# Kernel tuning notes

Measured on AMD Instinct MI355X. Metric: run time of the kernel, lower is better.

Reference implementation:

```python
import jax, jax.numpy as jnp
import numpy as np

N_NODES = 50000
N_EDGES = 1600000


def gcn_conv(h, W, b, src, dst, ew, n_nodes):
    """PyG GCNConv: linear -> add self-loops (weight 1) -> sym-norm scatter-add -> bias."""
    h = h @ W                                   # [N, out]
    loop = jnp.arange(n_nodes, dtype=src.dtype)
    s = jnp.concatenate([src, loop])            # [E+N]
    d = jnp.concatenate([dst, loop])
    w = jnp.concatenate([ew, jnp.ones((n_nodes,), dtype=h.dtype)])
    deg = jax.ops.segment_sum(w, d, num_segments=n_nodes)          # in-degree (weighted)
    dinv = jnp.where(deg > 0, jax.lax.rsqrt(deg), 0.0)
    coef = dinv[s] * w * dinv[d]                # D^-1/2 A D^-1/2 per-edge coefficient
    msg = h[s] * coef[:, None]                  # gather + scale  [E+N, out]
    out = jax.ops.segment_sum(msg, d, num_segments=n_nodes)        # scatter-add
    return out + b


def setup_inputs() -> dict:
    key = jax.random.key(0)
    ks = jax.random.split(key, 6)
    x = jax.random.normal(ks[0], (N_NODES, 256), dtype=jnp.float32)
    edge_index = jax.random.randint(ks[1], (2, N_EDGES), 0, N_NODES, dtype=jnp.int64)
    edge_weight = jax.random.uniform(ks[2], (N_EDGES,), dtype=jnp.float32)
    W1 = jax.random.normal(ks[3], (256, 128), dtype=jnp.float32) * (1.0 / np.sqrt(256))
    b1 = jnp.zeros((128,), dtype=jnp.float32)
    W2 = jax.random.normal(ks[4], (128, 64), dtype=jnp.float32) * (1.0 / np.sqrt(128))
    b2 = jnp.zeros((64,), dtype=jnp.float32)
    return {"x": x, "edge_index": edge_index, "edge_weight": edge_weight,
            "W1": W1, "b1": b1, "W2": W2, "b2": b2}


def reference(x, edge_index, edge_weight, W1, b1, W2, b2):
    src, dst = edge_index[0], edge_index[1]
    n = x.shape[0]
    h = gcn_conv(x, W1, b1, src, dst, edge_weight, n)
    h = jax.nn.relu(h)
    # dropout is identity in eval mode
    out = gcn_conv(h, W2, b2, src, dst, edge_weight, n)
    return out
```

## Files before the change

kernel.cpp:

```cpp
#include <hip/hip_runtime.h>

#define NN 50000
#define NE 1600000
#define NB 391
#define NBLK 512
#define EPB 3125
#define CAP 4608

typedef short bf16x8 __attribute__((ext_vector_type(8)));
typedef float f32x4 __attribute__((ext_vector_type(4)));

static __device__ __forceinline__ unsigned f2bf(float f) {
    union { float f; unsigned u; } v; v.f = f;
    return (v.u + 0x7FFF + ((v.u >> 16) & 1)) >> 16;
}

__global__ __launch_bounds__(256) void k1_scatter(const int* __restrict__ src,
        const int* __restrict__ dst, const float* __restrict__ ew,
        int* __restrict__ cursor, int2* __restrict__ ebuf,
        const float* __restrict__ W1, const float* __restrict__ W2,
        ushort* __restrict__ Wt1, ushort* __restrict__ Wt2) {
    int blk = blockIdx.x;
    int t = threadIdx.x;
    if (blk >= NBLK) {
        for (int idx = (blk - NBLK) * 256 + t; idx < 40960; idx += 32 * 256) {
            if (idx < 32768) {
                int k = idx >> 7, n = idx & 127;
                Wt1[n * 256 + k] = (ushort)f2bf(W1[idx]);
            } else {
                int i = idx - 32768;
                int k = i >> 6, n = i & 63;
                Wt2[n * 128 + k] = (ushort)f2bf(W2[i]);
            }
        }
        return;
    }
    __shared__ int h[NB];
    __shared__ int curs[NB];
    for (int i = t; i < NB; i += 256) h[i] = 0;
    __syncthreads();
    int base = blk * EPB;
    for (int k = t; k < EPB; k += 256)
        atomicAdd(&h[dst[base + k] >> 7], 1);
    __syncthreads();
    for (int i = t; i < NB; i += 256)
        curs[i] = i * CAP + atomicAdd(&cursor[i], h[i]);
    __syncthreads();
    for (int k = t; k < EPB; k += 256) {
        int d = dst[base + k];
        int s = src[base + k];
        float w = ew[base + k];
        int pos = atomicAdd(&curs[d >> 7], 1);
        ebuf[pos] = make_int2(s | ((d & 127) << 16), __float_as_int(w));
    }
}

__global__ __launch_bounds__(512) void p4_build(const int2* __restrict__ ebuf,
        const int* __restrict__ cursor, unsigned* __restrict__ edata,
        float* __restrict__ dinv, int2* __restrict__ rowptr2) {
    __shared__ int cnt[128], loff[128], cur[128], sd[128];
    __shared__ float deg[128];
    __shared__ int2 se[CAP];
    int bk = blockIdx.x;
    int t = threadIdx.x;
    int ebase = bk * CAP;
    int ecnt = cursor[bk];
    if (ecnt > CAP) ecnt = CAP;
    if (t < 128) { cnt[t] = 0; cur[t] = 0; deg[t] = 0.0f; }
    __syncthreads();
    for (int i = t; i < ecnt; i += 512) {
        int2 e = ebuf[ebase + i];
        se[i] = e;
        int dl = (e.x >> 16) & 127;
        atomicAdd(&cnt[dl], 1);
        atomicAdd(&deg[dl], __int_as_float(e.y));
    }
    __syncthreads();
    if (t < 128) sd[t] = cnt[t];
    __syncthreads();
    for (int off = 1; off < 128; off <<= 1) {
        int v = 0;
        if (t < 128 && t >= off) v = sd[t - off];
        __syncthreads();
        if (t < 128) sd[t] += v;
        __syncthreads();
    }
    if (t < 128) loff[t] = sd[t] - cnt[t];
    __syncthreads();
    int node = bk * 128 + t;
    if (t < 128 && node < NN) {
        dinv[node] = rsqrtf(deg[t] + 1.0f);
        int beg = ebase + loff[t];
        rowptr2[node] = make_int2(beg, beg + cnt[t]);
    }
    for (int i = t; i < ecnt; i += 512) {
        int2 e = se[i];
        int dl = (e.x >> 16) & 127;
        int slot = loff[dl] + atomicAdd(&cur[dl], 1);
        edata[ebase + slot] = (unsigned)(e.x & 0xFFFF)
                            | (f2bf(__int_as_float(e.y)) << 16);
    }
}

__global__ __launch_bounds__(256) void gemm1_kernel(const float* __restrict__ A,
        const ushort* __restrict__ Bt, ushort* __restrict__ C,
        const float* __restrict__ dinv, int M) {
    const int K = 256, N = 128;
    __shared__ __align__(16) ushort As[64][72];
    __shared__ __align__(16) ushort Bs[128][72];
    int tid = threadIdx.x;
    int bm = blockIdx.x * 64;
    int w = tid >> 6, lane = tid & 63;
    int m = lane & 15, quad = lane >> 4;
    f32x4 acc[8] = {};
    int ra = tid >> 2, ksa = (tid & 3) * 16;
    int rb = tid >> 1, ksb = (tid & 1) * 32;
    int grow = bm + ra; if (grow >= M) grow = M - 1;
    const float* ap = A + (size_t)grow * K + ksa;
    const ushort* bp = Bt + (size_t)rb * K + ksb;
    for (int k0 = 0; k0 < K; k0 += 64) {
        float4 f0 = *(const float4*)(ap + k0);
        float4 f1 = *(const float4*)(ap + k0 + 4);
        float4 f2 = *(const float4*)(ap + k0 + 8);
        float4 f3 = *(const float4*)(ap + k0 + 12);
        uint4 bv0 = *(const uint4*)(bp + k0);
        uint4 bv1 = *(const uint4*)(bp + k0 + 8);
        uint4 bv2 = *(const uint4*)(bp + k0 + 16);
        uint4 bv3 = *(const uint4*)(bp + k0 + 24);
        uint4 pa, pb;
        pa.x = f2bf(f0.x) | (f2bf(f0.y) << 16);
        pa.y = f2bf(f0.z) | (f2bf(f0.w) << 16);
        pa.z = f2bf(f1.x) | (f2bf(f1.y) << 16);
        pa.w = f2bf(f1.z) | (f2bf(f1.w) << 16);
        pb.x = f2bf(f2.x) | (f2bf(f2.y) << 16);
        pb.y = f2bf(f2.z) | (f2bf(f2.w) << 16);
        pb.z = f2bf(f3.x) | (f2bf(f3.y) << 16);
        pb.w = f2bf(f3.z) | (f2bf(f3.w) << 16);
        __syncthreads();
        *(uint4*)&As[ra][ksa] = pa;
        *(uint4*)&As[ra][ksa + 8] = pb;
        *(uint4*)&Bs[rb][ksb] = bv0;
        *(uint4*)&Bs[rb][ksb + 8] = bv1;
        *(uint4*)&Bs[rb][ksb + 16] = bv2;
        *(uint4*)&Bs[rb][ksb + 24] = bv3;
        __syncthreads();
        #pragma unroll
        for (int ks = 0; ks < 2; ++ks) {
            bf16x8 a = *(const bf16x8*)&As[w * 16 + m][ks * 32 + quad * 8];
            #pragma unroll
            for (int t = 0; t < 8; ++t) {
                bf16x8 b = *(const bf16x8*)&Bs[t * 16 + m][ks * 32 + quad * 8];
                acc[t] = __builtin_amdgcn_mfma_f32_16x16x32_bf16(a, b, acc[t], 0, 0, 0);
            }
        }
    }
    int rbase = bm + w * 16 + quad * 4;
    float dv[4];
    #pragma unroll
    for (int rg = 0; rg < 4; ++rg)
        dv[rg] = (rbase + rg < M) ? dinv[rbase + rg] : 0.0f;
    #pragma unroll
    for (int t = 0; t < 8; ++t) {
        int col = t * 16 + m;
        #pragma unroll
        for (int rg = 0; rg < 4; ++rg) {
            int row = rbase + rg;
            if (row < M)
                C[(size_t)row * N + col] = (ushort)f2bf(dv[rg] * acc[t][rg]);
        }
    }
}

__global__ __launch_bounds__(256) void agg1_fused_kernel(
        const int2* __restrict__ rowptr2, const unsigned* __restrict__ edata,
        const ushort* __restrict__ H, const float* __restrict__ dinv,
        const float* __restrict__ bias, const ushort* __restrict__ Wt2,
        ushort* __restrict__ H2) {
    __shared__ __align__(16) ushort Ats[16][136];
    int tid = threadIdx.x;
    int nl = tid >> 4;
    int node = blockIdx.x * 16 + nl;
    int glane = tid & 15;
    int gb = (tid & 63) & ~15;
    int2 rp = rowptr2[node];
    int beg = rp.x, end = rp.y;
    float acc[8] = {};
    const ushort* Hl = H + (size_t)glane * 8;
    for (int chunk = beg; chunk < end; chunk += 16) {
        int nch = end - chunk; if (nch > 16) nch = 16;
        int ed = 0;
        if (glane < nch) ed = (int)edata[chunk + glane];
        int j = 0;
        for (; j + 2 <= nch; j += 2) {
            int e0 = __shfl(ed, gb + j);
            int e1 = __shfl(ed, gb + j + 1);
            int s0 = e0 & 0xFFFF;
            int s1 = e1 & 0xFFFF;
            float c0 = __uint_as_float((unsigned)e0 & 0xFFFF0000u);
            float c1 = __uint_as_float((unsigned)e1 & 0xFFFF0000u);
            uint4 h0 = *(const uint4*)(Hl + (size_t)s0 * 128);
            uint4 h1 = *(const uint4*)(Hl + (size_t)s1 * 128);
            const unsigned* u0 = (const unsigned*)&h0;
            const unsigned* u1 = (const unsigned*)&h1;
            #pragma unroll
            for (int q = 0; q < 4; ++q) {
                acc[2*q]   += __uint_as_float(u0[q] << 16) * c0;
                acc[2*q+1] += __uint_as_float(u0[q] & 0xFFFF0000u) * c0;
            }
            #pragma unroll
            for (int q = 0; q < 4; ++q) {
                acc[2*q]   += __uint_as_float(u1[q] << 16) * c1;
                acc[2*q+1] += __uint_as_float(u1[q] & 0xFFFF0000u) * c1;
            }
        }
        if (j < nch) {
            int e0 = __shfl(ed, gb + j);
            int s0 = e0 & 0xFFFF;
            float c0 = __uint_as_float((unsigned)e0 & 0xFFFF0000u);
            uint4 h0 = *(const uint4*)(Hl + (size_t)s0 * 128);
            const unsigned* u0 = (const unsigned*)&h0;
            #pragma unroll
            for (int q = 0; q < 4; ++q) {
                acc[2*q]   += __uint_as_float(u0[q] << 16) * c0;
                acc[2*q+1] += __uint_as_float(u0[q] & 0xFFFF0000u) * c0;
            }
        }
    }
    float di = dinv[node];
    uint4 hn = *(const uint4*)(Hl + (size_t)node * 128);
    const unsigned* un = (const unsigned*)&hn;
    float4 bv0 = *(const float4*)(bias + glane * 8);
    float4 bv1 = *(const float4*)(bias + glane * 8 + 4);
    float v[8];
    #pragma unroll
    for (int q = 0; q < 4; ++q) {
        v[2*q]   = di * (acc[2*q]   + __uint_as_float(un[q] << 16));
        v[2*q+1] = di * (acc[2*q+1] + __uint_as_float(un[q] & 0xFFFF0000u));
    }
    v[0] += bv0.x; v[1] += bv0.y; v[2] += bv0.z; v[3] += bv0.w;
    v[4] += bv1.x; v[5] += bv1.y; v[6] += bv1.z; v[7] += bv1.w;
    #pragma unroll
    for (int k = 0; k < 8; ++k) v[k] = fmaxf(v[k], 0.0f);
    uint4 o;
    o.x = f2bf(v[0]) | (f2bf(v[1]) << 16);
    o.y = f2bf(v[2]) | (f2bf(v[3]) << 16);
    o.z = f2bf(v[4]) | (f2bf(v[5]) << 16);
    o.w = f2bf(v[6]) | (f2bf(v[7]) << 16);
    *(uint4*)&Ats[nl][glane * 8] = o;
    __syncthreads();
    int w = tid >> 6, lane = tid & 63;
    int m = lane & 15, quad = lane >> 4;
    const ushort* bp = Wt2 + (size_t)(w * 16 + m) * 128 + quad * 8;
    f32x4 c2 = {};
    #pragma unroll
    for (int kc = 0; kc < 4; ++kc) {
        bf16x8 a = *(const bf16x8*)&Ats[m][kc * 32 + quad * 8];
        bf16x8 b = *(const bf16x8*)(bp + kc * 32);
        c2 = __builtin_amdgcn_mfma_f32_16x16x32_bf16(a, b, c2, 0, 0, 0);
    }
    int rbase = blockIdx.x * 16 + quad * 4;
    #pragma unroll
    for (int rg = 0; rg < 4; ++rg) {
        float dvr = dinv[rbase + rg];
        H2[(size_t)(rbase + rg) * 64 + w * 16 + m] = (ushort)f2bf(dvr * c2[rg]);
    }
}

__global__ __launch_bounds__(256) void agg2_kernel(
        const int2* __restrict__ rowptr2, const unsigned* __restrict__ edata,
        const ushort* __restrict__ H, const float* __restrict__ dinv,
        const float* __restrict__ bias, float* __restrict__ out) {
    int node = blockIdx.x * 32 + (threadIdx.x >> 3);
    if (node >= NN) return;
    int glane = threadIdx.x & 7;
    int gb = (threadIdx.x & 63) & ~7;
    int2 rp = rowptr2[node];
    int beg = rp.x, end = rp.y;
    float acc[8] = {};
    const ushort* Hl = H + (size_t)glane * 8;
    for (int chunk = beg; chunk < end; chunk += 8) {
        int nch = end - chunk; if (nch > 8) nch = 8;
        int ed = 0;
        if (glane < nch) ed = (int)edata[chunk + glane];
        int j = 0;
        for (; j + 2 <= nch; j += 2) {
            int e0 = __shfl(ed, gb + j);
            int e1 = __shfl(ed, gb + j + 1);
            int s0 = e0 & 0xFFFF;
            int s1 = e1 & 0xFFFF;
            float c0 = __uint_as_float((unsigned)e0 & 0xFFFF0000u);
            float c1 = __uint_as_float((unsigned)e1 & 0xFFFF0000u);
            uint4 h0 = *(const uint4*)(Hl + (size_t)s0 * 64);
            uint4 h1 = *(const uint4*)(Hl + (size_t)s1 * 64);
            const unsigned* u0 = (const unsigned*)&h0;
            const unsigned* u1 = (const unsigned*)&h1;
            #pragma unroll
            for (int q = 0; q < 4; ++q) {
                acc[2*q]   += __uint_as_float(u0[q] << 16) * c0;
                acc[2*q+1] += __uint_as_float(u0[q] & 0xFFFF0000u) * c0;
            }
            #pragma unroll
            for (int q = 0; q < 4; ++q) {
                acc[2*q]   += __uint_as_float(u1[q] << 16) * c1;
                acc[2*q+1] += __uint_as_float(u1[q] & 0xFFFF0000u) * c1;
            }
        }
        if (j < nch) {
            int e0 = __shfl(ed, gb + j);
            int s0 = e0 & 0xFFFF;
            float c0 = __uint_as_float((unsigned)e0 & 0xFFFF0000u);
            uint4 h0 = *(const uint4*)(Hl + (size_t)s0 * 64);
            const unsigned* u0 = (const unsigned*)&h0;
            #pragma unroll
            for (int q = 0; q < 4; ++q) {
                acc[2*q]   += __uint_as_float(u0[q] << 16) * c0;
                acc[2*q+1] += __uint_as_float(u0[q] & 0xFFFF0000u) * c0;
            }
        }
    }
    float di = dinv[node];
    uint4 hn = *(const uint4*)(Hl + (size_t)node * 64);
    const unsigned* un = (const unsigned*)&hn;
    float4 bv0 = *(const float4*)(bias + glane * 8);
    float4 bv1 = *(const float4*)(bias + glane * 8 + 4);
    float v[8];
    #pragma unroll
    for (int q = 0; q < 4; ++q) {
        v[2*q]   = di * (acc[2*q]   + __uint_as_float(un[q] << 16));
        v[2*q+1] = di * (acc[2*q+1] + __uint_as_float(un[q] & 0xFFFF0000u));
    }
    v[0] += bv0.x; v[1] += bv0.y; v[2] += bv0.z; v[3] += bv0.w;
    v[4] += bv1.x; v[5] += bv1.y; v[6] += bv1.z; v[7] += bv1.w;
    float* o = out + (size_t)node * 64 + glane * 8;
    *(float4*)(o)     = make_float4(v[0], v[1], v[2], v[3]);
    *(float4*)(o + 4) = make_float4(v[4], v[5], v[6], v[7]);
}

extern "C" void kernel_launch(void* const* d_in, const int* in_sizes, int n_in,
                              void* d_out, int out_size, void* d_ws, size_t ws_size,
                              hipStream_t stream) {
    const float* x  = (const float*)d_in[0];
    const int*   ei = (const int*)d_in[1];
    const float* ew = (const float*)d_in[2];
    const float* W1 = (const float*)d_in[3];
    const float* b1 = (const float*)d_in[4];
    const float* W2 = (const float*)d_in[5];
    const float* b2 = (const float*)d_in[6];
    const int* src = ei;
    const int* dst = ei + NE;
    float* out = (float*)d_out;

    float*  ws      = (float*)d_ws;
    float*  dinv    = ws;
    int2*   rowptr2 = (int2*)(ws + 50048);
    int*    cursor  = (int*)(ws + 150144);
    ushort* Wt1     = (ushort*)(ws + 150656);
    ushort* Wt2     = Wt1 + 32768;
    unsigned* edata = (unsigned*)(ws + 171136);
    ushort* H1      = (ushort*)(ws + 1977472);
    ushort* H2      = (ushort*)(ws + 5177472);
    int2*   ebuf    = (int2*)H1;

    hipMemsetAsync(cursor, 0, NB * sizeof(int), stream);
    k1_scatter<<<NBLK + 32, 256, 0, stream>>>(src, dst, ew, cursor, ebuf,
                                              W1, W2, Wt1, Wt2);
    p4_build<<<NB, 512, 0, stream>>>(ebuf, cursor, edata, dinv, rowptr2);

    gemm1_kernel<<<782, 256, 0, stream>>>(x, Wt1, H1, dinv, NN);
    agg1_fused_kernel<<<3125, 256, 0, stream>>>(rowptr2, edata, H1, dinv, b1, Wt2, H2);
    agg2_kernel<<<1563, 256, 0, stream>>>(rowptr2, edata, H2, dinv, b2, out);
}
```

Before: 246.3 us.

## Pad CSR rows to multiples of four and unroll aggregation gathers by eight

Each destination row in the edge list is padded to a multiple of four with zero entries. The padding points at node 0 with weight 0, so it adds nothing to the sum. The aggregation kernels drop the per-chunk shuffle broadcast of edge data. Each lane now loads edge words directly and issues eight independent row gathers per iteration, which raises memory-level parallelism and removes tail handling. The scatter kernel also caches dst in shared memory to avoid a second global read. CAP and the workspace offsets grow to hold the padding, at the cost of a little extra zero-weight gather traffic.

```diff
diff --git a/kernel.cpp b/kernel.cpp
--- a/kernel.cpp
+++ b/kernel.cpp
@@ -5,7 +5,7 @@
 #define NB 391
 #define NBLK 512
 #define EPB 3125
-#define CAP 4608
+#define CAP 4992
 
 typedef short bf16x8 __attribute__((ext_vector_type(8)));
 typedef float f32x4 __attribute__((ext_vector_type(4)));
@@ -13,6 +13,15 @@
 static __device__ __forceinline__ unsigned f2bf(float f) {
     union { float f; unsigned u; } v; v.f = f;
     return (v.u + 0x7FFF + ((v.u >> 16) & 1)) >> 16;
+}
+
+static __device__ __forceinline__ void acc8(float* acc, uint4 h, float c) {
+    const unsigned* u = (const unsigned*)&h;
+    #pragma unroll
+    for (int q = 0; q < 4; ++q) {
+        acc[2*q]   += __uint_as_float(u[q] << 16) * c;
+        acc[2*q+1] += __uint_as_float(u[q] & 0xFFFF0000u) * c;
+    }
 }
 
 __global__ __launch_bounds__(256) void k1_scatter(const int* __restrict__ src,
@@ -37,17 +46,21 @@
     }
     __shared__ int h[NB];
     __shared__ int curs[NB];
+    __shared__ int sdst[EPB];
     for (int i = t; i < NB; i += 256) h[i] = 0;
     __syncthreads();
     int base = blk * EPB;
-    for (int k = t; k < EPB; k += 256)
-        atomicAdd(&h[dst[base + k] >> 7], 1);
+    for (int k = t; k < EPB; k += 256) {
+        int d = dst[base + k];
+        sdst[k] = d;
+        atomicAdd(&h[d >> 7], 1);
+    }
     __syncthreads();
     for (int i = t; i < NB; i += 256)
         curs[i] = i * CAP + atomicAdd(&cursor[i], h[i]);
     __syncthreads();
     for (int k = t; k < EPB; k += 256) {
-        int d = dst[base + k];
+        int d = sdst[k];
         int s = src[base + k];
         float w = ew[base + k];
         int pos = atomicAdd(&curs[d >> 7], 1);
@@ -76,7 +89,7 @@
         atomicAdd(&deg[dl], __int_as_float(e.y));
     }
     __syncthreads();
-    if (t < 128) sd[t] = cnt[t];
+    if (t < 128) sd[t] = (cnt[t] + 3) & ~3;
     __syncthreads();
     for (int off = 1; off < 128; off <<= 1) {
         int v = 0;
@@ -85,13 +98,19 @@
         if (t < 128) sd[t] += v;
         __syncthreads();
     }
-    if (t < 128) loff[t] = sd[t] - cnt[t];
+    if (t < 128) {
+        int cp = (cnt[t] + 3) & ~3;
+        loff[t] = sd[t] - cp;
+    }
     __syncthreads();
     int node = bk * 128 + t;
     if (t < 128 && node < NN) {
         dinv[node] = rsqrtf(deg[t] + 1.0f);
+        int cp = (cnt[t] + 3) & ~3;
         int beg = ebase + loff[t];
-        rowptr2[node] = make_int2(beg, beg + cnt[t]);
+        rowptr2[node] = make_int2(beg, beg + cp);
+        for (int i = cnt[t]; i < cp; ++i)
+            edata[ebase + loff[t] + i] = 0;
     }
     for (int i = t; i < ecnt; i += 512) {
         int2 e = se[i];
@@ -181,50 +200,51 @@
     int nl = tid >> 4;
     int node = blockIdx.x * 16 + nl;
     int glane = tid & 15;
-    int gb = (tid & 63) & ~15;
     int2 rp = rowptr2[node];
     int beg = rp.x, end = rp.y;
     float acc[8] = {};
     const ushort* Hl = H + (size_t)glane * 8;
-    for (int chunk = beg; chunk < end; chunk += 16) {
-        int nch = end - chunk; if (nch > 16) nch = 16;
-        int ed = 0;
-        if (glane < nch) ed = (int)edata[chunk + glane];
-        int j = 0;
-        for (; j + 2 <= nch; j += 2) {
-            int e0 = __shfl(ed, gb + j);
-            int e1 = __shfl(ed, gb + j + 1);
-            int s0 = e0 & 0xFFFF;
-            int s1 = e1 & 0xFFFF;
-            float c0 = __uint_as_float((unsigned)e0 & 0xFFFF0000u);
-            float c1 = __uint_as_float((unsigned)e1 & 0xFFFF0000u);
-            uint4 h0 = *(const uint4*)(Hl + (size_t)s0 * 128);
-            uint4 h1 = *(const uint4*)(Hl + (size_t)s1 * 128);
-            const unsigned* u0 = (const unsigned*)&h0;
-            const unsigned* u1 = (const unsigned*)&h1;
-            #pragma unroll
-            for (int q = 0; q < 4; ++q) {
-                acc[2*q]   += __uint_as_float(u0[q] << 16) * c0;
-                acc[2*q+1] += __uint_as_float(u0[q] & 0xFFFF0000u) * c0;
-            }
-            #pragma unroll
-            for (int q = 0; q < 4; ++q) {
-                acc[2*q]   += __uint_as_float(u1[q] << 16) * c1;
-                acc[2*q+1] += __uint_as_float(u1[q] & 0xFFFF0000u) * c1;
-            }
-        }
-        if (j < nch) {
-            int e0 = __shfl(ed, gb + j);
-            int s0 = e0 & 0xFFFF;
-            float c0 = __uint_as_float((unsigned)e0 & 0xFFFF0000u);
-            uint4 h0 = *(const uint4*)(Hl + (size_t)s0 * 128);
-            const unsigned* u0 = (const unsigned*)&h0;
-            #pragma unroll
-            for (int q = 0; q < 4; ++q) {
-                acc[2*q]   += __uint_as_float(u0[q] << 16) * c0;
-                acc[2*q+1] += __uint_as_float(u0[q] & 0xFFFF0000u) * c0;
-            }
-        }
+    int e = beg;
+    int n8 = beg + ((end - beg) & ~7);
+    for (; e < n8; e += 8) {
+        unsigned m0 = edata[e];
+        unsigned m1 = edata[e + 1];
+        unsigned m2 = edata[e + 2];
+        unsigned m3 = edata[e + 3];
+        unsigned m4 = edata[e + 4];
+        unsigned m5 = edata[e + 5];
+        unsigned m6 = edata[e + 6];
+        unsigned m7 = edata[e + 7];
+        uint4 h0 = *(const uint4*)(Hl + (size_t)(m0 & 0xFFFF) * 128);
+        uint4 h1 = *(const uint4*)(Hl + (size_t)(m1 & 0xFFFF) * 128);
+        uint4 h2 = *(const uint4*)(Hl + (size_t)(m2 & 0xFFFF) * 128);
+        uint4 h3 = *(const uint4*)(Hl + (size_t)(m3 & 0xFFFF) * 128);
+        uint4 h4 = *(const uint4*)(Hl + (size_t)(m4 & 0xFFFF) * 128);
+        uint4 h5 = *(const uint4*)(Hl + (size_t)(m5 & 0xFFFF) * 128);
+        uint4 h6 = *(const uint4*)(Hl + (size_t)(m6 & 0xFFFF) * 128);
+        uint4 h7 = *(const uint4*)(Hl + (size_t)(m7 & 0xFFFF) * 128);
+        acc8(acc, h0, __uint_as_float(m0 & 0xFFFF0000u));
+        acc8(acc, h1, __uint_as_float(m1 & 0xFFFF0000u));
+        acc8(acc, h2, __uint_as_float(m2 & 0xFFFF0000u));
+        acc8(acc, h3, __uint_as_float(m3 & 0xFFFF0000u));
+        acc8(acc, h4, __uint_as_float(m4 & 0xFFFF0000u));
+        acc8(acc, h5, __uint_as_float(m5 & 0xFFFF0000u));
+        acc8(acc, h6, __uint_as_float(m6 & 0xFFFF0000u));
+        acc8(acc, h7, __uint_as_float(m7 & 0xFFFF0000u));
+    }
+    if (e < end) {
+        unsigned m0 = edata[e];
+        unsigned m1 = edata[e + 1];
+        unsigned m2 = edata[e + 2];
+        unsigned m3 = edata[e + 3];
+        uint4 h0 = *(const uint4*)(Hl + (size_t)(m0 & 0xFFFF) * 128);
+        uint4 h1 = *(const uint4*)(Hl + (size_t)(m1 & 0xFFFF) * 128);
+        uint4 h2 = *(const uint4*)(Hl + (size_t)(m2 & 0xFFFF) * 128);
+        uint4 h3 = *(const uint4*)(Hl + (size_t)(m3 & 0xFFFF) * 128);
+        acc8(acc, h0, __uint_as_float(m0 & 0xFFFF0000u));
+        acc8(acc, h1, __uint_as_float(m1 & 0xFFFF0000u));
+        acc8(acc, h2, __uint_as_float(m2 & 0xFFFF0000u));
+        acc8(acc, h3, __uint_as_float(m3 & 0xFFFF0000u));
     }
     float di = dinv[node];
     uint4 hn = *(const uint4*)(Hl + (size_t)node * 128);
@@ -273,50 +293,51 @@
     int node = blockIdx.x * 32 + (threadIdx.x >> 3);
     if (node >= NN) return;
     int glane = threadIdx.x & 7;
-    int gb = (threadIdx.x & 63) & ~7;
     int2 rp = rowptr2[node];
     int beg = rp.x, end = rp.y;
     float acc[8] = {};
     const ushort* Hl = H + (size_t)glane * 8;
-    for (int chunk = beg; chunk < end; chunk += 8) {
-        int nch = end - chunk; if (nch > 8) nch = 8;
-        int ed = 0;
-        if (glane < nch) ed = (int)edata[chunk + glane];
-        int j = 0;
-        for (; j + 2 <= nch; j += 2) {
-            int e0 = __shfl(ed, gb + j);
-            int e1 = __shfl(ed, gb + j + 1);
-            int s0 = e0 & 0xFFFF;
-            int s1 = e1 & 0xFFFF;
-            float c0 = __uint_as_float((unsigned)e0 & 0xFFFF0000u);
-            float c1 = __uint_as_float((unsigned)e1 & 0xFFFF0000u);
-            uint4 h0 = *(const uint4*)(Hl + (size_t)s0 * 64);
-            uint4 h1 = *(const uint4*)(Hl + (size_t)s1 * 64);
-            const unsigned* u0 = (const unsigned*)&h0;
-            const unsigned* u1 = (const unsigned*)&h1;
-            #pragma unroll
-            for (int q = 0; q < 4; ++q) {
-                acc[2*q]   += __uint_as_float(u0[q] << 16) * c0;
-                acc[2*q+1] += __uint_as_float(u0[q] & 0xFFFF0000u) * c0;
-            }
-            #pragma unroll
-            for (int q = 0; q < 4; ++q) {
-                acc[2*q]   += __uint_as_float(u1[q] << 16) * c1;
-                acc[2*q+1] += __uint_as_float(u1[q] & 0xFFFF0000u) * c1;
-            }
-        }
-        if (j < nch) {
-            int e0 = __shfl(ed, gb + j);
-            int s0 = e0 & 0xFFFF;
-            float c0 = __uint_as_float((unsigned)e0 & 0xFFFF0000u);
-            uint4 h0 = *(const uint4*)(Hl + (size_t)s0 * 64);
-            const unsigned* u0 = (const unsigned*)&h0;
-            #pragma unroll
-            for (int q = 0; q < 4; ++q) {
-                acc[2*q]   += __uint_as_float(u0[q] << 16) * c0;
-                acc[2*q+1] += __uint_as_float(u0[q] & 0xFFFF0000u) * c0;
-            }
-        }
+    int e = beg;
+    int n8 = beg + ((end - beg) & ~7);
+    for (; e < n8; e += 8) {
+        unsigned m0 = edata[e];
+        unsigned m1 = edata[e + 1];
+        unsigned m2 = edata[e + 2];
+        unsigned m3 = edata[e + 3];
+        unsigned m4 = edata[e + 4];
+        unsigned m5 = edata[e + 5];
+        unsigned m6 = edata[e + 6];
+        unsigned m7 = edata[e + 7];
+        uint4 h0 = *(const uint4*)(Hl + (size_t)(m0 & 0xFFFF) * 64);
+        uint4 h1 = *(const uint4*)(Hl + (size_t)(m1 & 0xFFFF) * 64);
+        uint4 h2 = *(const uint4*)(Hl + (size_t)(m2 & 0xFFFF) * 64);
+        uint4 h3 = *(const uint4*)(Hl + (size_t)(m3 & 0xFFFF) * 64);
+        uint4 h4 = *(const uint4*)(Hl + (size_t)(m4 & 0xFFFF) * 64);
+        uint4 h5 = *(const uint4*)(Hl + (size_t)(m5 & 0xFFFF) * 64);
+        uint4 h6 = *(const uint4*)(Hl + (size_t)(m6 & 0xFFFF) * 64);
+        uint4 h7 = *(const uint4*)(Hl + (size_t)(m7 & 0xFFFF) * 64);
+        acc8(acc, h0, __uint_as_float(m0 & 0xFFFF0000u));
+        acc8(acc, h1, __uint_as_float(m1 & 0xFFFF0000u));
+        acc8(acc, h2, __uint_as_float(m2 & 0xFFFF0000u));
+        acc8(acc, h3, __uint_as_float(m3 & 0xFFFF0000u));
+        acc8(acc, h4, __uint_as_float(m4 & 0xFFFF0000u));
+        acc8(acc, h5, __uint_as_float(m5 & 0xFFFF0000u));
+        acc8(acc, h6, __uint_as_float(m6 & 0xFFFF0000u));
+        acc8(acc, h7, __uint_as_float(m7 & 0xFFFF0000u));
+    }
+    if (e < end) {
+        unsigned m0 = edata[e];
+        unsigned m1 = edata[e + 1];
+        unsigned m2 = edata[e + 2];
+        unsigned m3 = edata[e + 3];
+        uint4 h0 = *(const uint4*)(Hl + (size_t)(m0 & 0xFFFF) * 64);
+        uint4 h1 = *(const uint4*)(Hl + (size_t)(m1 & 0xFFFF) * 64);
+        uint4 h2 = *(const uint4*)(Hl + (size_t)(m2 & 0xFFFF) * 64);
+        uint4 h3 = *(const uint4*)(Hl + (size_t)(m3 & 0xFFFF) * 64);
+        acc8(acc, h0, __uint_as_float(m0 & 0xFFFF0000u));
+        acc8(acc, h1, __uint_as_float(m1 & 0xFFFF0000u));
+        acc8(acc, h2, __uint_as_float(m2 & 0xFFFF0000u));
+        acc8(acc, h3, __uint_as_float(m3 & 0xFFFF0000u));
     }
     float di = dinv[node];
     uint4 hn = *(const uint4*)(Hl + (size_t)node * 64);
@@ -357,8 +378,8 @@
     ushort* Wt1     = (ushort*)(ws + 150656);
     ushort* Wt2     = Wt1 + 32768;
     unsigned* edata = (unsigned*)(ws + 171136);
-    ushort* H1      = (ushort*)(ws + 1977472);
-    ushort* H2      = (ushort*)(ws + 5177472);
+    ushort* H1      = (ushort*)(ws + 2123008);
+    ushort* H2      = (ushort*)(ws + 5323008);
     int2*   ebuf    = (int2*)H1;
 
     hipMemsetAsync(cursor, 0, NB * sizeof(int), stream);
```

New measurement: 245.2 us. Within noise of the previous version (-0.5%).
